# Kernel optimization log

Hardware: AMD Instinct MI355X
Metric: run time of the kernel (lower is better)

## Reference

```python
import jax, jax.numpy as jnp
import numpy as np

EPS = 1e-5

def _inorm(t, axes):
    m = t.mean(axis=axes, keepdims=True)
    v = t.var(axis=axes, keepdims=True)
    return (t - m) * jax.lax.rsqrt(v + EPS)

def setup_inputs() -> dict:
    key = jax.random.key(0)
    ks = jax.random.split(key, 7)
    b, c, d, o, h, w = 2, 128, 128, 128, 16, 16
    maxlen = 256
    return {
        "x": jax.random.normal(ks[0], (b, c, h, w), jnp.float32),
        "y": jax.random.normal(ks[1], (b, d, h, w), jnp.float32),
        "pos_emb": jax.random.normal(ks[2], (maxlen, c), jnp.float32) * 0.02,
        "w1": jax.random.normal(ks[3], (o, 2 * c + d), jnp.float32) * 0.05,
        "b1": jax.random.normal(ks[4], (o,), jnp.float32) * 0.01,
        "w2": jax.random.normal(ks[5], (o, o), jnp.float32) * 0.05,
        "b2": jax.random.normal(ks[6], (o,), jnp.float32) * 0.01,
    }

def reference(x, y, pos_emb, w1, b1, w2, b2):
    b, c, h, w = x.shape
    d = y.shape[1]
    hw = h * w
    # positional embedding: tokens = arange(hw), permute to channel-first
    pos = pos_emb[:hw].T.reshape(c, h, w)  # [c,h,w]
    x = x + pos[None]
    x = jax.nn.relu(_inorm(x, (2, 3)))
    y = jax.nn.relu(_inorm(y, (2, 3)))
    xf = x.reshape(b, c, hw)
    yf = y.reshape(b, d, hw)
    # conv1x1 over cat([x_i, x_j, y]) splits into three GEMMs (same math):
    Wi, Wj, Wy = w1[:, :c], w1[:, c:2 * c], w1[:, 2 * c:]
    A = jnp.einsum('oc,bcj->boj', Wi, xf)                    # varies along j
    B = jnp.einsum('oc,bci->boi', Wj, xf) + jnp.einsum('od,bdi->boi', Wy, yf)  # varies along i
    z = A[:, :, None, :] + B[:, :, :, None] + b1[None, :, None, None]  # [b,o,hw,hw]
    z = jax.nn.relu(_inorm(z, (2, 3)))
    # second conv1x1 then sum over dim=3 commutes: w2 @ sum_j z + hw*b2
    s = z.sum(axis=3)  # [b,o,hw]
    out = jnp.einsum('po,boi->bpi', w2, s) + hw * b2[None, :, None]
    return out.reshape(b, -1, h, w)
```

## Files before the change

### kernel.cpp

```cpp
#include <hip/hip_runtime.h>

#define HW 256
#define C  128

template<int NW>
__device__ __forceinline__ void blockReduce4(float& a, float& b, float& c, float& d,
                                             float (*sm)[4]) {
    #pragma unroll
    for (int off = 32; off > 0; off >>= 1) {
        a += __shfl_xor(a, off, 64);
        b += __shfl_xor(b, off, 64);
        c += __shfl_xor(c, off, 64);
        d += __shfl_xor(d, off, 64);
    }
    const int wid  = threadIdx.x >> 6;
    const int lane = threadIdx.x & 63;
    if (lane == 0) { sm[wid][0] = a; sm[wid][1] = b; sm[wid][2] = c; sm[wid][3] = d; }
    __syncthreads();
    a = 0.f; b = 0.f; c = 0.f; d = 0.f;
    #pragma unroll
    for (int w = 0; w < NW; ++w) {
        a += sm[w][0]; b += sm[w][1]; c += sm[w][2]; d += sm[w][3];
    }
    __syncthreads();
}

__global__ __launch_bounds__(256) void k_norm(
        const float* __restrict__ x, const float* __restrict__ y,
        const float* __restrict__ pos, float* __restrict__ xn, float* __restrict__ yn) {
    __shared__ float sm[4][4];
    const int blk = blockIdx.x;
    const int tid = threadIdx.x;
    float v;
    float* dst;
    if (blk < 256) {
        const int c = blk & 127;
        v = x[blk * HW + tid] + pos[tid * C + c];
        dst = xn + blk * HW;
    } else {
        const int bc = blk - 256;
        v = y[bc * HW + tid];
        dst = yn + bc * HW;
    }
    float s = v, s2 = v * v, z3 = 0.f, z4 = 0.f;
    blockReduce4<4>(s, s2, z3, z4, sm);
    const float m   = s  * (1.0f / 256.0f);
    const float var = s2 * (1.0f / 256.0f) - m * m;
    const float r   = (v - m) * rsqrtf(var + 1e-5f);
    dst[tid] = r > 0.0f ? r : 0.0f;
}

__global__ __launch_bounds__(1024) void k_rel(
        const float* __restrict__ xn, const float* __restrict__ yn,
        const float* __restrict__ w1, float* __restrict__ s_out) {
    __shared__ float pA[4][256];
    __shared__ float pB[4][256];
    __shared__ float red[16][4];
    __shared__ float aj[256];
    __shared__ float bi[256];
    __shared__ float wrow[384];

    const int t  = threadIdx.x;
    const int i  = t & 255;
    const int q  = t >> 8;
    const int bo = blockIdx.x;
    const int b  = bo >> 7;
    const int o  = bo & 127;

    if (t < 384) wrow[t] = w1[o * 384 + t];
    __syncthreads();

    const float* xb = xn + b * (C * HW);
    const float* yb = yn + b * (C * HW);

    float A = 0.f, Bv = 0.f;
    const int c0 = q * 32;
    #pragma unroll
    for (int cc = 0; cc < 32; ++cc) {
        const int c = c0 + cc;
        const float xv = xb[c * HW + i];
        A  = fmaf(wrow[c],       xv, A);
        Bv = fmaf(wrow[128 + c], xv, Bv);
        const float yv = yb[c * HW + i];
        Bv = fmaf(wrow[256 + c], yv, Bv);
    }
    pA[q][i] = A;
    pB[q][i] = Bv;
    __syncthreads();

    float Af = 0.f, Bf = 0.f;
    if (t < 256) {
        Af = pA[0][i] + pA[1][i] + pA[2][i] + pA[3][i];
        Bf = pB[0][i] + pB[1][i] + pB[2][i] + pB[3][i];
    }
    float sA = Af, sA2 = Af * Af, sB = Bf, sB2 = Bf * Bf;
    blockReduce4<16>(sA, sA2, sB, sB2, red);

    const float mA   = sA  * (1.0f / 256.0f);
    const float mB   = sB  * (1.0f / 256.0f);
    const float varA = sA2 * (1.0f / 256.0f) - mA * mA;
    const float varB = sB2 * (1.0f / 256.0f) - mB * mB;
    const float istd = rsqrtf(varA + varB + 1e-5f);

    if (t < 256) {
        aj[i] = (Af - mA) * istd;
        bi[i] = (Bf - mB) * istd;
    }
    __syncthreads();

    const float bb = bi[i];
    float acc = 0.f;
    const int j0 = q * 64;
    #pragma unroll
    for (int jj = 0; jj < 64; ++jj) {
        const float v = aj[j0 + jj] + bb;
        acc += (v > 0.f ? v : 0.f);
    }
    pA[q][i] = acc;
    __syncthreads();
    if (t < 256)
        s_out[bo * HW + i] = pA[0][i] + pA[1][i] + pA[2][i] + pA[3][i];
}

__global__ __launch_bounds__(1024) void k_out(
        const float* __restrict__ s_in, const float* __restrict__ w2,
        const float* __restrict__ b2, float* __restrict__ out) {
    __shared__ float wrow[128];
    __shared__ float pacc[4][256];
    const int t  = threadIdx.x;
    const int i  = t & 255;
    const int q  = t >> 8;
    const int bp = blockIdx.x;
    const int b  = bp >> 7;
    const int p  = bp & 127;
    if (t < 128) wrow[t] = w2[p * 128 + t];
    __syncthreads();
    const float* sb = s_in + b * (C * HW);
    float acc = 0.f;
    const int o0 = q * 32;
    #pragma unroll
    for (int oo = 0; oo < 32; ++oo)
        acc = fmaf(wrow[o0 + oo], sb[(o0 + oo) * HW + i], acc);
    pacc[q][i] = acc;
    __syncthreads();
    if (t < 256)
        out[bp * HW + i] = pacc[0][i] + pacc[1][i] + pacc[2][i] + pacc[3][i]
                           + 256.0f * b2[p];
}

extern "C" void kernel_launch(void* const* d_in, const int* in_sizes, int n_in,
                              void* d_out, int out_size, void* d_ws, size_t ws_size,
                              hipStream_t stream) {
    const float* x   = (const float*)d_in[0];
    const float* y   = (const float*)d_in[1];
    const float* pos = (const float*)d_in[2];
    const float* w1  = (const float*)d_in[3];
    const float* w2  = (const float*)d_in[5];
    const float* b2  = (const float*)d_in[6];
    float* out = (float*)d_out;

    float* xn = (float*)d_ws;
    float* yn = xn + 65536;
    float* s  = yn + 65536;

    k_norm<<<512, 256, 0, stream>>>(x, y, pos, xn, yn);
    k_rel <<<256, 1024, 0, stream>>>(xn, yn, w1, s);
    k_out <<<256, 1024, 0, stream>>>(s, w2, b2, out);
}
```

Baseline: 77.75 us.

## Fuse norm, relation and output kernels into one cooperative kernel with grid syncs

Replaces three separate launches with a single cooperative kernel of 256 blocks x 1024 threads, using grid.sync between the normalization, pairwise relation, and output GEMM phases. Each block normalizes two channel rows in phase one. This removes two kernel launch gaps and inter-kernel drain, at the cost of grid-wide barrier overhead and requiring all 256 large blocks to be co-resident.

```diff
diff --git a/kernel.cpp b/kernel.cpp
--- a/kernel.cpp
+++ b/kernel.cpp
@@ -1,58 +1,19 @@
 #include <hip/hip_runtime.h>
+#include <hip/hip_cooperative_groups.h>
+
+namespace cg = cooperative_groups;
 
 #define HW 256
 #define C  128
 
-template<int NW>
-__device__ __forceinline__ void blockReduce4(float& a, float& b, float& c, float& d,
-                                             float (*sm)[4]) {
-    #pragma unroll
-    for (int off = 32; off > 0; off >>= 1) {
-        a += __shfl_xor(a, off, 64);
-        b += __shfl_xor(b, off, 64);
-        c += __shfl_xor(c, off, 64);
-        d += __shfl_xor(d, off, 64);
-    }
-    const int wid  = threadIdx.x >> 6;
-    const int lane = threadIdx.x & 63;
-    if (lane == 0) { sm[wid][0] = a; sm[wid][1] = b; sm[wid][2] = c; sm[wid][3] = d; }
-    __syncthreads();
-    a = 0.f; b = 0.f; c = 0.f; d = 0.f;
-    #pragma unroll
-    for (int w = 0; w < NW; ++w) {
-        a += sm[w][0]; b += sm[w][1]; c += sm[w][2]; d += sm[w][3];
-    }
-    __syncthreads();
-}
+__global__ __launch_bounds__(1024) void k_fused(
+        const float* __restrict__ x, const float* __restrict__ y,
+        const float* __restrict__ pos, const float* __restrict__ w1,
+        const float* __restrict__ w2, const float* __restrict__ b2,
+        float* __restrict__ xn, float* __restrict__ yn,
+        float* __restrict__ sbuf, float* __restrict__ out) {
+    cg::grid_group grid = cg::this_grid();
 
-__global__ __launch_bounds__(256) void k_norm(
-        const float* __restrict__ x, const float* __restrict__ y,
-        const float* __restrict__ pos, float* __restrict__ xn, float* __restrict__ yn) {
-    __shared__ float sm[4][4];
-    const int blk = blockIdx.x;
-    const int tid = threadIdx.x;
-    float v;
-    float* dst;
-    if (blk < 256) {
-        const int c = blk & 127;
-        v = x[blk * HW + tid] + pos[tid * C + c];
-        dst = xn + blk * HW;
-    } else {
-        const int bc = blk - 256;
-        v = y[bc * HW + tid];
-        dst = yn + bc * HW;
-    }
-    float s = v, s2 = v * v, z3 = 0.f, z4 = 0.f;
-    blockReduce4<4>(s, s2, z3, z4, sm);
-    const float m   = s  * (1.0f / 256.0f);
-    const float var = s2 * (1.0f / 256.0f) - m * m;
-    const float r   = (v - m) * rsqrtf(var + 1e-5f);
-    dst[tid] = r > 0.0f ? r : 0.0f;
-}
-
-__global__ __launch_bounds__(1024) void k_rel(
-        const float* __restrict__ xn, const float* __restrict__ yn,
-        const float* __restrict__ w1, float* __restrict__ s_out) {
     __shared__ float pA[4][256];
     __shared__ float pB[4][256];
     __shared__ float red[16][4];
@@ -60,92 +21,132 @@
     __shared__ float bi[256];
     __shared__ float wrow[384];
 
-    const int t  = threadIdx.x;
-    const int i  = t & 255;
-    const int q  = t >> 8;
-    const int bo = blockIdx.x;
-    const int b  = bo >> 7;
-    const int o  = bo & 127;
+    const int t    = threadIdx.x;
+    const int blk  = blockIdx.x;
+    const int g    = t >> 8;
+    const int l    = t & 255;
+    const int wgl  = t >> 6;
+    const int lane = t & 63;
 
+    float v = 0.0f;
+    float* dstA = nullptr;
+    if (g < 2) {
+        const int jb = blk * 2 + g;
+        if (jb < 256) {
+            const int c = jb & 127;
+            v = x[jb * HW + l] + pos[l * C + c];
+            dstA = xn + jb * HW;
+        } else {
+            const int bc = jb - 256;
+            v = y[bc * HW + l];
+            dstA = yn + bc * HW;
+        }
+    }
+    float s1 = v, s2 = v * v;
+    #pragma unroll
+    for (int off = 32; off > 0; off >>= 1) {
+        s1 += __shfl_xor(s1, off, 64);
+        s2 += __shfl_xor(s2, off, 64);
+    }
+    if (lane == 0) { red[wgl][0] = s1; red[wgl][1] = s2; }
+    __syncthreads();
+    if (g < 2) {
+        const int w0 = g * 4;
+        const float S1 = red[w0][0] + red[w0+1][0] + red[w0+2][0] + red[w0+3][0];
+        const float S2 = red[w0][1] + red[w0+1][1] + red[w0+2][1] + red[w0+3][1];
+        const float m   = S1 * (1.0f / 256.0f);
+        const float var = S2 * (1.0f / 256.0f) - m * m;
+        const float r   = (v - m) * rsqrtf(var + 1e-5f);
+        dstA[l] = r > 0.0f ? r : 0.0f;
+    }
+    __threadfence();
+    grid.sync();
+
+    const int b = blk >> 7;
+    const int o = blk & 127;
     if (t < 384) wrow[t] = w1[o * 384 + t];
     __syncthreads();
 
     const float* xb = xn + b * (C * HW);
     const float* yb = yn + b * (C * HW);
 
-    float A = 0.f, Bv = 0.f;
-    const int c0 = q * 32;
+    float A = 0.0f, Bv = 0.0f;
+    const int c0 = g * 32;
     #pragma unroll
     for (int cc = 0; cc < 32; ++cc) {
         const int c = c0 + cc;
-        const float xv = xb[c * HW + i];
+        const float xv = xb[c * HW + l];
         A  = fmaf(wrow[c],       xv, A);
         Bv = fmaf(wrow[128 + c], xv, Bv);
-        const float yv = yb[c * HW + i];
+        const float yv = yb[c * HW + l];
         Bv = fmaf(wrow[256 + c], yv, Bv);
     }
-    pA[q][i] = A;
-    pB[q][i] = Bv;
+    pA[g][l] = A;
+    pB[g][l] = Bv;
     __syncthreads();
 
-    float Af = 0.f, Bf = 0.f;
+    float Af = 0.0f, Bf = 0.0f;
     if (t < 256) {
-        Af = pA[0][i] + pA[1][i] + pA[2][i] + pA[3][i];
-        Bf = pB[0][i] + pB[1][i] + pB[2][i] + pB[3][i];
+        Af = pA[0][l] + pA[1][l] + pA[2][l] + pA[3][l];
+        Bf = pB[0][l] + pB[1][l] + pB[2][l] + pB[3][l];
     }
-    float sA = Af, sA2 = Af * Af, sB = Bf, sB2 = Bf * Bf;
-    blockReduce4<16>(sA, sA2, sB, sB2, red);
-
+    float rA = Af, rA2 = Af * Af, rB = Bf, rB2 = Bf * Bf;
+    #pragma unroll
+    for (int off = 32; off > 0; off >>= 1) {
+        rA  += __shfl_xor(rA,  off, 64);
+        rA2 += __shfl_xor(rA2, off, 64);
+        rB  += __shfl_xor(rB,  off, 64);
+        rB2 += __shfl_xor(rB2, off, 64);
+    }
+    if (lane == 0) { red[wgl][0] = rA; red[wgl][1] = rA2; red[wgl][2] = rB; red[wgl][3] = rB2; }
+    __syncthreads();
+    float sA = 0.f, sA2 = 0.f, sB = 0.f, sB2 = 0.f;
+    #pragma unroll
+    for (int w = 0; w < 16; ++w) {
+        sA += red[w][0]; sA2 += red[w][1]; sB += red[w][2]; sB2 += red[w][3];
+    }
     const float mA   = sA  * (1.0f / 256.0f);
     const float mB   = sB  * (1.0f / 256.0f);
     const float varA = sA2 * (1.0f / 256.0f) - mA * mA;
     const float varB = sB2 * (1.0f / 256.0f) - mB * mB;
     const float istd = rsqrtf(varA + varB + 1e-5f);
 
+    __syncthreads();
     if (t < 256) {
-        aj[i] = (Af - mA) * istd;
-        bi[i] = (Bf - mB) * istd;
+        aj[l] = (Af - mA) * istd;
+        bi[l] = (Bf - mB) * istd;
     }
     __syncthreads();
 
-    const float bb = bi[i];
-    float acc = 0.f;
-    const int j0 = q * 64;
+    const float bb = bi[l];
+    float acc = 0.0f;
+    const int j0 = g * 64;
     #pragma unroll
     for (int jj = 0; jj < 64; ++jj) {
-        const float v = aj[j0 + jj] + bb;
-        acc += (v > 0.f ? v : 0.f);
+        const float zv = aj[j0 + jj] + bb;
+        acc += (zv > 0.0f ? zv : 0.0f);
     }
-    pA[q][i] = acc;
+    pA[g][l] = acc;
     __syncthreads();
     if (t < 256)
-        s_out[bo * HW + i] = pA[0][i] + pA[1][i] + pA[2][i] + pA[3][i];
-}
+        sbuf[blk * HW + l] = pA[0][l] + pA[1][l] + pA[2][l] + pA[3][l];
+    __threadfence();
+    grid.sync();
 
-__global__ __launch_bounds__(1024) void k_out(
-        const float* __restrict__ s_in, const float* __restrict__ w2,
-        const float* __restrict__ b2, float* __restrict__ out) {
-    __shared__ float wrow[128];
-    __shared__ float pacc[4][256];
-    const int t  = threadIdx.x;
-    const int i  = t & 255;
-    const int q  = t >> 8;
-    const int bp = blockIdx.x;
-    const int b  = bp >> 7;
-    const int p  = bp & 127;
+    const int p = blk & 127;
     if (t < 128) wrow[t] = w2[p * 128 + t];
     __syncthreads();
-    const float* sb = s_in + b * (C * HW);
-    float acc = 0.f;
-    const int o0 = q * 32;
+    const float* sb = sbuf + b * (C * HW);
+    float acc2 = 0.0f;
+    const int o0 = g * 32;
     #pragma unroll
     for (int oo = 0; oo < 32; ++oo)
-        acc = fmaf(wrow[o0 + oo], sb[(o0 + oo) * HW + i], acc);
-    pacc[q][i] = acc;
+        acc2 = fmaf(wrow[o0 + oo], sb[(o0 + oo) * HW + l], acc2);
+    pB[g][l] = acc2;
     __syncthreads();
     if (t < 256)
-        out[bp * HW + i] = pacc[0][i] + pacc[1][i] + pacc[2][i] + pacc[3][i]
-                           + 256.0f * b2[p];
+        out[blk * HW + l] = pB[0][l] + pB[1][l] + pB[2][l] + pB[3][l]
+                            + 256.0f * b2[p];
 }
 
 extern "C" void kernel_launch(void* const* d_in, const int* in_sizes, int n_in,
@@ -161,9 +162,11 @@
 
     float* xn = (float*)d_ws;
     float* yn = xn + 65536;
-    float* s  = yn + 65536;
+    float* sb = yn + 65536;
 
-    k_norm<<<512, 256, 0, stream>>>(x, y, pos, xn, yn);
-    k_rel <<<256, 1024, 0, stream>>>(xn, yn, w1, s);
-    k_out <<<256, 1024, 0, stream>>>(s, w2, b2, out);
+    void* args[] = { (void*)&x, (void*)&y, (void*)&pos, (void*)&w1,
+                     (void*)&w2, (void*)&b2,
+                     (void*)&xn, (void*)&yn, (void*)&sb, (void*)&out };
+    hipLaunchCooperativeKernel((const void*)k_fused, dim3(256), dim3(1024),
+                               args, 0, stream);
 }
```

Result: slower. 283.5 us (+264.6%).
